# Kernel tuning notes

Hardware: AMD Instinct MI355X
Metric: run time of the kernel (lower is better)

Reference implementation:

```python
import jax, jax.numpy as jnp
import numpy as np

B, S, D, H = 2, 2048, 1024, 16
HD = D // H
DFF = 4096
EPS = 1e-5


def layernorm(x, w, b):
    m = jnp.mean(x, axis=-1, keepdims=True)
    v = jnp.mean((x - m) ** 2, axis=-1, keepdims=True)
    return (x - m) / jnp.sqrt(v + EPS) * w + b


def setup_inputs() -> dict:
    key = jax.random.key(0)
    ks = jax.random.split(key, 5)
    s = 0.02  # init scale for weights
    return {
        "src": jax.random.normal(ks[0], (B, S, D), jnp.float32),
        "norm_w": jnp.ones((D,), jnp.float32),
        "norm_b": jnp.zeros((D,), jnp.float32),
        "wqkv_w": jax.random.normal(ks[1], (D, 3 * D), jnp.float32) * s,
        "wqkv_b": jnp.zeros((3 * D,), jnp.float32),
        "out_w": jax.random.normal(ks[2], (D, D), jnp.float32) * s,
        "out_b": jnp.zeros((D,), jnp.float32),
        "fnorm_w": jnp.ones((D,), jnp.float32),
        "fnorm_b": jnp.zeros((D,), jnp.float32),
        "ff1_w": jax.random.normal(ks[3], (D, DFF), jnp.float32) * s,
        "ff1_b": jnp.zeros((DFF,), jnp.float32),
        "ff2_w": jax.random.normal(ks[4], (DFF, D), jnp.float32) * s,
        "ff2_b": jnp.zeros((D,), jnp.float32),
    }


def reference(src, norm_w, norm_b, wqkv_w, wqkv_b, out_w, out_b,
              fnorm_w, fnorm_b, ff1_w, ff1_b, ff2_w, ff2_b):
    bs, seq, dim = src.shape
    hd = dim // H
    qkv = layernorm(src, norm_w, norm_b) @ wqkv_w + wqkv_b  # [b,s,3d]
    qkv = qkv.reshape(bs, seq, 3, H, hd).transpose(2, 0, 3, 1, 4)  # [3,b,h,s,hd]
    q, k, v = qkv[0], qkv[1], qkv[2]
    # ALiBi bias: (j - i) * 2^{-h}, -inf above diagonal (causal)
    i = jnp.arange(seq)[:, None]
    j = jnp.arange(seq)[None, :]
    slopes = 2.0 ** (-jnp.arange(H, dtype=jnp.float32))  # [h]
    rel = (j - i).astype(jnp.float32)  # [s,s]
    bias = slopes[:, None, None] * rel[None]  # [h,s,s]
    bias = jnp.where((j > i)[None], -jnp.inf, bias)
    scale = 1.0 / jnp.sqrt(jnp.asarray(hd, jnp.float32))
    scores = jnp.einsum("bhqd,bhkd->bhqk", q, k) * scale + bias[None]
    attn = jax.nn.softmax(scores, axis=-1)
    ctx = jnp.einsum("bhqk,bhkd->bhqd", attn, v)
    ctx = ctx.transpose(0, 2, 1, 3).reshape(bs, seq, dim)
    src = src + ctx @ out_w + out_b
    h = layernorm(src, fnorm_w, fnorm_b)
    ff = jax.nn.relu(h @ ff1_w + ff1_b) @ ff2_w + ff2_b
    return src + ff
```

## Files before the change

kernel.cpp:

```cpp
#include <hip/hip_runtime.h>
#include <math.h>

#define S_   2048
#define D_   1024
#define H_   16
#define DFF_ 4096

#define NEGINF (-__builtin_huge_valf())

typedef __bf16 bf16x8 __attribute__((ext_vector_type(8)));
typedef __bf16 bf16x4 __attribute__((ext_vector_type(4)));
typedef float  f32x4  __attribute__((ext_vector_type(4)));

static __device__ __forceinline__ unsigned short f2bf_rne(float f) {
    unsigned int u = __float_as_uint(f);
    u = (u + 0x7fffu + ((u >> 16) & 1u)) >> 16;
    return (unsigned short)u;
}

template<bool OBF>
__global__ __launch_bounds__(256) void ln_kernel(
    const float* __restrict__ x, const float* __restrict__ w,
    const float* __restrict__ b, void* __restrict__ y)
{
    const int row = blockIdx.x;
    const int t = threadIdx.x;
    const float4 v = reinterpret_cast<const float4*>(x + (size_t)row * D_)[t];
    float s  = v.x + v.y + v.z + v.w;
    float ss = v.x*v.x + v.y*v.y + v.z*v.z + v.w*v.w;
    #pragma unroll
    for (int o = 32; o; o >>= 1) {
        s  += __shfl_xor(s,  o, 64);
        ss += __shfl_xor(ss, o, 64);
    }
    __shared__ float red[8];
    const int wid = t >> 6, lane = t & 63;
    if (lane == 0) { red[wid] = s; red[4 + wid] = ss; }
    __syncthreads();
    s  = red[0] + red[1] + red[2] + red[3];
    ss = red[4] + red[5] + red[6] + red[7];
    const float mean = s * (1.f / D_);
    const float var  = ss * (1.f / D_) - mean * mean;
    const float rstd = rsqrtf(var + 1e-5f);
    const float4 wv = reinterpret_cast<const float4*>(w)[t];
    const float4 bv = reinterpret_cast<const float4*>(b)[t];
    float4 o;
    o.x = (v.x - mean) * rstd * wv.x + bv.x;
    o.y = (v.y - mean) * rstd * wv.y + bv.y;
    o.z = (v.z - mean) * rstd * wv.z + bv.z;
    o.w = (v.w - mean) * rstd * wv.w + bv.w;
    if (OBF) {
        ushort4 o4;
        o4.x = f2bf_rne(o.x); o4.y = f2bf_rne(o.y);
        o4.z = f2bf_rne(o.z); o4.w = f2bf_rne(o.w);
        reinterpret_cast<ushort4*>((unsigned short*)y + (size_t)row * D_)[t] = o4;
    } else {
        reinterpret_cast<float4*>((float*)y + (size_t)row * D_)[t] = o;
    }
}

__global__ __launch_bounds__(256) void wcast_kernel(
    const float* __restrict__ in, unsigned short* __restrict__ outT, int K, int N)
{
    __shared__ float t[64][65];
    const int n0 = blockIdx.x * 64, k0 = blockIdx.y * 64;
    const int tid = threadIdx.x;
    #pragma unroll
    for (int i = 0; i < 16; ++i) {
        const int idx = i * 256 + tid;
        const int kk = idx >> 6, nn = idx & 63;
        t[kk][nn] = in[(size_t)(k0 + kk) * N + n0 + nn];
    }
    __syncthreads();
    #pragma unroll
    for (int i = 0; i < 16; ++i) {
        const int idx = i * 256 + tid;
        const int nn = idx >> 6, kk = idx & 63;
        outT[(size_t)(n0 + nn) * K + k0 + kk] = f2bf_rne(t[kk][nn]);
    }
}

template<int EPI, bool OBF, int BN>
__global__ __launch_bounds__(256) void bgemm_kernel(
    const __bf16* __restrict__ A,
    const __bf16* __restrict__ Bt,
    const float* __restrict__ bias, const float* __restrict__ res,
    void* __restrict__ Cv, int M, int N, int K)
{
    constexpr int B_IT = BN / 32;
    constexpr int MI   = (BN == 128) ? 4 : 2;
    __shared__ __align__(16) __bf16 As[2][128 * 64];
    __shared__ __align__(16) __bf16 Bs[2][BN * 64];
    const int tid  = threadIdx.x;
    const int w    = tid >> 6, lane = tid & 63;
    const int wrow0 = (BN == 128) ? (w >> 1) * 64 : w * 32;
    const int wcol0 = (BN == 128) ? (w & 1) * 64 : 0;

    const int nwg  = gridDim.x;
    const int lin  = blockIdx.x;
    const int wg   = (lin & 7) * (nwg >> 3) + (lin >> 3);
    const int gridM = M >> 7;
    const int col0 = (wg / gridM) * BN;
    const int row0 = (wg % gridM) << 7;

    const int srow = lane >> 3;
    const int scol = ((lane & 7) ^ srow) << 3;
    const int frow = lane & 15;
    const int l4   = lane >> 4;
    const int r7   = frow & 7;

    const __bf16* Abase = A  + (size_t)(row0 + srow) * K + scol;
    const __bf16* Bbase = Bt + (size_t)(col0 + srow) * K + scol;

    f32x4 acc[MI][4] = {};
    const int nt = K >> 6;

#define STAGE_G(bufi, kt)                                                              \
    _Pragma("unroll")                                                                  \
    for (int it = 0; it < 4; ++it) {                                                   \
        const int arow = w * 32 + it * 8;                                              \
        __builtin_amdgcn_global_load_lds(                                              \
            (__attribute__((address_space(1))) void*)(Abase + (size_t)arow * K + (kt)),\
            (__attribute__((address_space(3))) void*)(&As[bufi][arow * 64]), 16, 0, 0);\
    }                                                                                  \
    _Pragma("unroll")                                                                  \
    for (int it = 0; it < B_IT; ++it) {                                                \
        const int brow = w * (BN / 4) + it * 8;                                        \
        __builtin_amdgcn_global_load_lds(                                              \
            (__attribute__((address_space(1))) void*)(Bbase + (size_t)brow * K + (kt)),\
            (__attribute__((address_space(3))) void*)(&Bs[bufi][brow * 64]), 16, 0, 0);\
    }

    STAGE_G(0, 0)
    int buf = 0;
    for (int t = 0; t < nt; ++t) {
        __syncthreads();
        if (t + 1 < nt) {
            STAGE_G(buf ^ 1, (t + 1) << 6)
        }
        #pragma unroll
        for (int kk = 0; kk < 2; ++kk) {
            const int ch = ((kk * 4 + l4) ^ r7) * 8;
            bf16x8 af[MI], bfr[4];
            #pragma unroll
            for (int i = 0; i < MI; ++i)
                af[i] = *(const bf16x8*)&As[buf][(wrow0 + i * 16 + frow) * 64 + ch];
            #pragma unroll
            for (int i = 0; i < 4; ++i)
                bfr[i] = *(const bf16x8*)&Bs[buf][(wcol0 + i * 16 + frow) * 64 + ch];
            #pragma unroll
            for (int mi = 0; mi < MI; ++mi)
                #pragma unroll
                for (int ni = 0; ni < 4; ++ni)
                    acc[mi][ni] = __builtin_amdgcn_mfma_f32_16x16x32_bf16(
                        af[mi], bfr[ni], acc[mi][ni], 0, 0, 0);
        }
        buf ^= 1;
    }
#undef STAGE_G

    float bz[4];
    #pragma unroll
    for (int ni = 0; ni < 4; ++ni) bz[ni] = bias[col0 + wcol0 + ni * 16 + frow];
    #pragma unroll
    for (int mi = 0; mi < MI; ++mi) {
        #pragma unroll
        for (int j = 0; j < 4; ++j) {
            const int row = row0 + wrow0 + mi * 16 + l4 * 4 + j;
            #pragma unroll
            for (int ni = 0; ni < 4; ++ni) {
                const int col = col0 + wcol0 + ni * 16 + frow;
                float v = acc[mi][ni][j] + bz[ni];
                if (EPI == 1) v = fmaxf(v, 0.f);
                if (EPI == 2) v += res[(size_t)row * N + col];
                if (OBF) ((unsigned short*)Cv)[(size_t)row * N + col] = f2bf_rne(v);
                else     ((float*)Cv)[(size_t)row * N + col] = v;
            }
        }
    }
}

__global__ __launch_bounds__(256) void attn_kernel(
    const __bf16* __restrict__ qkv, __bf16* __restrict__ ctx)
{
    const int bh   = blockIdx.x & 31;
    const int qt   = 31 - (blockIdx.x >> 5);
    const int b    = bh >> 4, h = bh & 15;
    const int tid  = threadIdx.x;
    const int wid  = tid >> 6, lane = tid & 63;
    const int l15  = lane & 15, l4 = lane >> 4;
    const float slope2 = exp2f(-(float)h) * 1.44269504f;
    const size_t rowb = (size_t)b * S_;

    __shared__ __align__(16) __bf16 Ks[64 * 72];
    __shared__ __align__(16) __bf16 Vt[64 * 72];
    __shared__ __align__(16) __bf16 Ps[4 * 16 * 72];

    const int jr = tid >> 3;
    const int c  = tid & 7;
    const int c8 = c * 8;
    __bf16* psw = &Ps[wid * 16 * 72];
    const __bf16* base = qkv + rowb * 3072 + h * 64;

    const int i0 = qt << 6;

    bf16x8 qf[2];
    {
        const float QSC = 0.125f * 1.44269504f;
        const __bf16* qp = base + (size_t)(i0 + wid * 16 + l15) * 3072 + l4 * 8;
        bf16x8 r0 = *(const bf16x8*)(qp);
        bf16x8 r1 = *(const bf16x8*)(qp + 32);
        #pragma unroll
        for (int e = 0; e < 8; ++e) {
            qf[0][e] = (__bf16)((float)r0[e] * QSC);
            qf[1][e] = (__bf16)((float)r1[e] * QSC);
        }
    }

    float cb[4][4];
    #pragma unroll
    for (int ni = 0; ni < 4; ++ni)
        #pragma unroll
        for (int j = 0; j < 4; ++j)
            cb[ni][j] = slope2 * (float)(ni * 16 + l4 * 4 + j - wid * 16 - l15);

    float lsum = 0.f;
    f32x4 acc[4];
    #pragma unroll
    for (int ni = 0; ni < 4; ++ni) acc[ni] = (f32x4){0.f, 0.f, 0.f, 0.f};

    bf16x8 k0, k1, v0, v1;
    {
        const __bf16* kvp = base + (size_t)jr * 3072;
        k0 = *(const bf16x8*)(kvp + 1024 + c8);
        v0 = *(const bf16x8*)(kvp + 2048 + c8);
        k1 = *(const bf16x8*)(kvp + 32 * 3072 + 1024 + c8);
        v1 = *(const bf16x8*)(kvp + 32 * 3072 + 2048 + c8);
    }

    for (int kt = 0; kt <= qt; ++kt) {
        __syncthreads();
        *(bf16x8*)&Ks[jr * 72 + c8]        = k0;
        *(bf16x8*)&Ks[(jr + 32) * 72 + c8] = k1;
        const int sw0 = (((jr >> 3) ^ c) & 7) * 8 + (jr & 7);
        const int sw1 = ((((jr + 32) >> 3) ^ c) & 7) * 8 + (jr & 7);
        #pragma unroll
        for (int e = 0; e < 8; ++e) {
            Vt[(c8 + e) * 72 + sw0] = v0[e];
            Vt[(c8 + e) * 72 + sw1] = v1[e];
        }
        __syncthreads();

        if (kt < qt) {
            const __bf16* kvp = base + (size_t)(((kt + 1) << 6) + jr) * 3072;
            k0 = *(const bf16x8*)(kvp + 1024 + c8);
            v0 = *(const bf16x8*)(kvp + 2048 + c8);
            k1 = *(const bf16x8*)(kvp + 32 * 3072 + 1024 + c8);
            v1 = *(const bf16x8*)(kvp + 32 * 3072 + 2048 + c8);
        }

        f32x4 sf[4];
        #pragma unroll
        for (int ni = 0; ni < 4; ++ni) sf[ni] = (f32x4){0.f, 0.f, 0.f, 0.f};
        #pragma unroll
        for (int kd = 0; kd < 2; ++kd)
            #pragma unroll
            for (int ni = 0; ni < 4; ++ni) {
                const bf16x8 kf = *(const bf16x8*)&Ks[(ni * 16 + l15) * 72 + kd * 32 + l4 * 8];
                sf[ni] = __builtin_amdgcn_mfma_f32_16x16x32_bf16(kf, qf[kd], sf[ni], 0, 0, 0);
            }

        float p[4][4];
        if (kt == qt) {
            #pragma unroll
            for (int ni = 0; ni < 4; ++ni)
                #pragma unroll
                for (int j = 0; j < 4; ++j) {
                    const float e = (cb[ni][j] > 0.f)
                        ? 0.f
                        : __builtin_amdgcn_exp2f(sf[ni][j] + cb[ni][j]);
                    p[ni][j] = e;
                    lsum += e;
                }
        } else {
            const float dstep = slope2 * (float)((kt << 6) - i0);
            #pragma unroll
            for (int ni = 0; ni < 4; ++ni)
                #pragma unroll
                for (int j = 0; j < 4; ++j) {
                    const float e = __builtin_amdgcn_exp2f(sf[ni][j] + (cb[ni][j] + dstep));
                    p[ni][j] = e;
                    lsum += e;
                }
        }

        #pragma unroll
        for (int ni = 0; ni < 4; ++ni) {
            bf16x4 pk;
            pk[0] = (__bf16)p[ni][0]; pk[1] = (__bf16)p[ni][1];
            pk[2] = (__bf16)p[ni][2]; pk[3] = (__bf16)p[ni][3];
            *(bf16x4*)&psw[l15 * 72 + ni * 16 + l4 * 4] = pk;
        }
        asm volatile("" ::: "memory");

        #pragma unroll
        for (int kk = 0; kk < 2; ++kk) {
            const bf16x8 pa = *(const bf16x8*)&psw[l15 * 72 + kk * 32 + l4 * 8];
            #pragma unroll
            for (int ni = 0; ni < 4; ++ni) {
                const int d = ni * 16 + l15;
                const int pc = ((kk * 4 + l4) ^ (d >> 3)) & 7;
                const bf16x8 bv = *(const bf16x8*)&Vt[d * 72 + pc * 8];
                acc[ni] = __builtin_amdgcn_mfma_f32_16x16x32_bf16(pa, bv, acc[ni], 0, 0, 0);
            }
        }
    }

    lsum += __shfl_xor(lsum, 16, 64);
    lsum += __shfl_xor(lsum, 32, 64);
    float linv[4];
    #pragma unroll
    for (int j = 0; j < 4; ++j)
        linv[j] = 1.f / __shfl(lsum, l4 * 4 + j, 64);

    #pragma unroll
    for (int ni = 0; ni < 4; ++ni) {
        const int col = h * 64 + ni * 16 + l15;
        #pragma unroll
        for (int j = 0; j < 4; ++j) {
            const int row = i0 + wid * 16 + l4 * 4 + j;
            ctx[(rowb + row) * (size_t)D_ + col] = (__bf16)(acc[ni][j] * linv[j]);
        }
    }
}

extern "C" void kernel_launch(void* const* d_in, const int* in_sizes, int n_in,
                              void* d_out, int out_size, void* d_ws, size_t ws_size,
                              hipStream_t stream) {
    const float* src     = (const float*)d_in[0];
    const float* norm_w  = (const float*)d_in[1];
    const float* norm_b  = (const float*)d_in[2];
    const float* wqkv_w  = (const float*)d_in[3];
    const float* wqkv_b  = (const float*)d_in[4];
    const float* out_w   = (const float*)d_in[5];
    const float* out_b   = (const float*)d_in[6];
    const float* fnorm_w = (const float*)d_in[7];
    const float* fnorm_b = (const float*)d_in[8];
    const float* ff1_w   = (const float*)d_in[9];
    const float* ff1_b   = (const float*)d_in[10];
    const float* ff2_w   = (const float*)d_in[11];
    const float* ff2_b   = (const float*)d_in[12];
    float* out = (float*)d_out;

    const int M = 2 * S_;
    const size_t MB = 1u << 20;
    char* W = (char*)d_ws;
    unsigned short* wqkvT = (unsigned short*)(W);
    unsigned short* outT  = (unsigned short*)(W + 6  * MB);
    unsigned short* ff1T  = (unsigned short*)(W + 8  * MB);
    unsigned short* ff2T  = (unsigned short*)(W + 16 * MB);
    unsigned short* h1    = (unsigned short*)(W + 24 * MB);
    unsigned short* qkv   = (unsigned short*)(W + 32 * MB);
    unsigned short* ctx   = (unsigned short*)(W + 24 * MB);
    unsigned short* h2    = (unsigned short*)(W + 32 * MB);
    unsigned short* ffmid = (unsigned short*)(W + 40 * MB);
    float*          src2  = (float*)        (W + 80 * MB);

    wcast_kernel<<<dim3(3072/64, 1024/64), 256, 0, stream>>>(wqkv_w, wqkvT, 1024, 3072);
    wcast_kernel<<<dim3(1024/64, 1024/64), 256, 0, stream>>>(out_w,  outT,  1024, 1024);
    wcast_kernel<<<dim3(4096/64, 1024/64), 256, 0, stream>>>(ff1_w,  ff1T,  1024, 4096);
    wcast_kernel<<<dim3(1024/64, 4096/64), 256, 0, stream>>>(ff2_w,  ff2T,  4096, 1024);

    ln_kernel<true><<<M, 256, 0, stream>>>(src, norm_w, norm_b, h1);
    bgemm_kernel<0, true, 128><<<(3072/128) * (M/128), 256, 0, stream>>>(
        (const __bf16*)h1, (const __bf16*)wqkvT, wqkv_b, nullptr, qkv, M, 3072, 1024);
    attn_kernel<<<1024, 256, 0, stream>>>((const __bf16*)qkv, (__bf16*)ctx);
    bgemm_kernel<2, false, 64><<<(1024/64) * (M/128), 256, 0, stream>>>(
        (const __bf16*)ctx, (const __bf16*)outT, out_b, src, src2, M, 1024, 1024);
    ln_kernel<true><<<M, 256, 0, stream>>>(src2, fnorm_w, fnorm_b, h2);
    bgemm_kernel<1, true, 128><<<(4096/128) * (M/128), 256, 0, stream>>>(
        (const __bf16*)h2, (const __bf16*)ff1T, ff1_b, nullptr, ffmid, M, 4096, 1024);
    bgemm_kernel<2, false, 64><<<(1024/64) * (M/128), 256, 0, stream>>>(
        (const __bf16*)ffmid, (const __bf16*)ff2T, ff2_b, src2, out, M, 1024, 4096);
}
```

Before: 344.5 us.

## Split-K the FF2 GEMM with reduction kernel and use BK=32 for wide GEMMs

The final FF2 GEMM (K=4096) now runs as a two-way split-K. Each half writes fp32 partials, and a separate ksum kernel adds the partials, the residual and the bias. This doubles the workgroup count so more CUs are busy. The GEMM kernel is also templated on the K-tile size, with BK=32 and an adjusted LDS swizzle used for the QKV and FF1 GEMMs, which cuts LDS use per block. The cost is extra fp32 traffic for the partials and one more kernel launch.

```diff
diff --git a/kernel.cpp b/kernel.cpp
--- a/kernel.cpp
+++ b/kernel.cpp
@@ -80,74 +80,89 @@
     }
 }
 
-template<int EPI, bool OBF, int BN>
+template<int EPI, bool OBF, int BN, int BK>
 __global__ __launch_bounds__(256) void bgemm_kernel(
     const __bf16* __restrict__ A,
     const __bf16* __restrict__ Bt,
     const float* __restrict__ bias, const float* __restrict__ res,
     void* __restrict__ Cv, int M, int N, int K)
 {
-    constexpr int B_IT = BN / 32;
-    constexpr int MI   = (BN == 128) ? 4 : 2;
-    __shared__ __align__(16) __bf16 As[2][128 * 64];
-    __shared__ __align__(16) __bf16 Bs[2][BN * 64];
+    constexpr int RPI = 512 / BK;
+    constexpr int NCH = BK / 8;
+    constexpr int AIT = 32 / RPI;
+    constexpr int BIT = (BN / 4) / RPI;
+    constexpr int MI  = (BN == 128) ? 4 : 2;
+    constexpr int KKN = BK / 32;
+
+    __shared__ __align__(16) __bf16 As[2][128 * BK];
+    __shared__ __align__(16) __bf16 Bs[2][BN * BK];
     const int tid  = threadIdx.x;
     const int w    = tid >> 6, lane = tid & 63;
     const int wrow0 = (BN == 128) ? (w >> 1) * 64 : w * 32;
     const int wcol0 = (BN == 128) ? (w & 1) * 64 : 0;
 
-    const int nwg  = gridDim.x;
-    const int lin  = blockIdx.x;
-    const int wg   = (lin & 7) * (nwg >> 3) + (lin >> 3);
+    const int lin = blockIdx.x;
+    const int wg_full = (lin & 7) * (gridDim.x >> 3) + (lin >> 3);
+    int wg = wg_full, ks = 0;
+    if (EPI == 3) {
+        const int half = gridDim.x >> 1;
+        ks = wg_full >= half;
+        wg = wg_full - ks * half;
+    }
     const int gridM = M >> 7;
     const int col0 = (wg / gridM) * BN;
     const int row0 = (wg % gridM) << 7;
-
-    const int srow = lane >> 3;
-    const int scol = ((lane & 7) ^ srow) << 3;
-    const int frow = lane & 15;
-    const int l4   = lane >> 4;
-    const int r7   = frow & 7;
-
-    const __bf16* Abase = A  + (size_t)(row0 + srow) * K + scol;
-    const __bf16* Bbase = Bt + (size_t)(col0 + srow) * K + scol;
+    const int Keff  = (EPI == 3) ? (K >> 1) : K;
+    const int kbase = ks * Keff;
+
+    const int srow   = lane / NCH;
+    const int schunk = lane % NCH;
+    const int swk_s  = (BK == 64) ? (srow & 7) : ((srow >> 1) & 3);
+    const int scol   = (schunk ^ swk_s) * 8;
+    const int frow   = lane & 15;
+    const int l4     = lane >> 4;
+    const int swk_r  = (BK == 64) ? (frow & 7) : ((frow >> 1) & 3);
+
+    const __bf16* Abase = A  + (size_t)(row0 + srow) * K + kbase + scol;
+    const __bf16* Bbase = Bt + (size_t)(col0 + srow) * K + kbase + scol;
 
     f32x4 acc[MI][4] = {};
-    const int nt = K >> 6;
-
-#define STAGE_G(bufi, kt)                                                              \
-    _Pragma("unroll")                                                                  \
-    for (int it = 0; it < 4; ++it) {                                                   \
-        const int arow = w * 32 + it * 8;                                              \
-        __builtin_amdgcn_global_load_lds(                                              \
-            (__attribute__((address_space(1))) void*)(Abase + (size_t)arow * K + (kt)),\
-            (__attribute__((address_space(3))) void*)(&As[bufi][arow * 64]), 16, 0, 0);\
-    }                                                                                  \
-    _Pragma("unroll")                                                                  \
-    for (int it = 0; it < B_IT; ++it) {                                                \
-        const int brow = w * (BN / 4) + it * 8;                                        \
-        __builtin_amdgcn_global_load_lds(                                              \
-            (__attribute__((address_space(1))) void*)(Bbase + (size_t)brow * K + (kt)),\
-            (__attribute__((address_space(3))) void*)(&Bs[bufi][brow * 64]), 16, 0, 0);\
-    }
-
-    STAGE_G(0, 0)
+    const int nt = Keff / BK;
+
+    auto STAGE = [&](int bufi, int kt) {
+        #pragma unroll
+        for (int it = 0; it < AIT; ++it) {
+            const int arow = w * 32 + it * RPI;
+            __builtin_amdgcn_global_load_lds(
+                (__attribute__((address_space(1))) void*)(Abase + (size_t)arow * K + kt),
+                (__attribute__((address_space(3))) void*)(&As[bufi][arow * BK]), 16, 0, 0);
+        }
+        #pragma unroll
+        for (int it = 0; it < BIT; ++it) {
+            const int brow = w * (BN / 4) + it * RPI;
+            __builtin_amdgcn_global_load_lds(
+                (__attribute__((address_space(1))) void*)(Bbase + (size_t)brow * K + kt),
+                (__attribute__((address_space(3))) void*)(&Bs[bufi][brow * BK]), 16, 0, 0);
+        }
+    };
+
+    STAGE(0, 0);
     int buf = 0;
     for (int t = 0; t < nt; ++t) {
         __syncthreads();
         if (t + 1 < nt) {
-            STAGE_G(buf ^ 1, (t + 1) << 6)
-        }
-        #pragma unroll
-        for (int kk = 0; kk < 2; ++kk) {
-            const int ch = ((kk * 4 + l4) ^ r7) * 8;
+            STAGE(buf ^ 1, (t + 1) * BK);
+        }
+        #pragma unroll
+        for (int kk = 0; kk < KKN; ++kk) {
+            const int ch = ((kk * 4 + l4) ^ swk_r) * 8;
             bf16x8 af[MI], bfr[4];
             #pragma unroll
             for (int i = 0; i < MI; ++i)
-                af[i] = *(const bf16x8*)&As[buf][(wrow0 + i * 16 + frow) * 64 + ch];
+                af[i] = *(const bf16x8*)&As[buf][(wrow0 + i * 16 + frow) * BK + ch];
             #pragma unroll
             for (int i = 0; i < 4; ++i)
-                bfr[i] = *(const bf16x8*)&Bs[buf][(wcol0 + i * 16 + frow) * 64 + ch];
+                bfr[i] = *(const bf16x8*)&Bs[buf][(wcol0 + i * 16 + frow) * BK + ch];
             #pragma unroll
             for (int mi = 0; mi < MI; ++mi)
                 #pragma unroll
@@ -157,11 +172,13 @@
         }
         buf ^= 1;
     }
-#undef STAGE_G
-
-    float bz[4];
-    #pragma unroll
-    for (int ni = 0; ni < 4; ++ni) bz[ni] = bias[col0 + wcol0 + ni * 16 + frow];
+
+    float bz[4] = {0.f, 0.f, 0.f, 0.f};
+    if (EPI != 3) {
+        #pragma unroll
+        for (int ni = 0; ni < 4; ++ni) bz[ni] = bias[col0 + wcol0 + ni * 16 + frow];
+    }
+    float* Cd = (EPI == 3) ? (ks ? (float*)res : (float*)Cv) : (float*)Cv;
     #pragma unroll
     for (int mi = 0; mi < MI; ++mi) {
         #pragma unroll
@@ -173,10 +190,32 @@
                 float v = acc[mi][ni][j] + bz[ni];
                 if (EPI == 1) v = fmaxf(v, 0.f);
                 if (EPI == 2) v += res[(size_t)row * N + col];
-                if (OBF) ((unsigned short*)Cv)[(size_t)row * N + col] = f2bf_rne(v);
-                else     ((float*)Cv)[(size_t)row * N + col] = v;
+                if (EPI == 3) Cd[(size_t)row * N + col] = v;
+                else if (OBF) ((unsigned short*)Cv)[(size_t)row * N + col] = f2bf_rne(v);
+                else          ((float*)Cv)[(size_t)row * N + col] = v;
             }
         }
+    }
+}
+
+__global__ __launch_bounds__(256) void ksum_kernel(
+    const float* __restrict__ p0, const float* __restrict__ p1,
+    const float* __restrict__ s2, const float* __restrict__ bias,
+    float* __restrict__ out)
+{
+    const int total = 4096 * 1024 / 4;
+    const int stride = gridDim.x * 256;
+    for (int i = blockIdx.x * 256 + threadIdx.x; i < total; i += stride) {
+        const float4 a  = ((const float4*)p0)[i];
+        const float4 b  = ((const float4*)p1)[i];
+        const float4 s  = ((const float4*)s2)[i];
+        const float4 bs = ((const float4*)bias)[i & 255];
+        float4 o;
+        o.x = s.x + a.x + b.x + bs.x;
+        o.y = s.y + a.y + b.y + bs.y;
+        o.z = s.z + a.z + b.z + bs.z;
+        o.w = s.w + a.w + b.w + bs.w;
+        ((float4*)out)[i] = o;
     }
 }
 
@@ -365,6 +404,8 @@
     unsigned short* h2    = (unsigned short*)(W + 32 * MB);
     unsigned short* ffmid = (unsigned short*)(W + 40 * MB);
     float*          src2  = (float*)        (W + 80 * MB);
+    float*          p0    = (float*)        (W + 24 * MB);
+    float*          p1    = (float*)        (W + 96 * MB);
 
     wcast_kernel<<<dim3(3072/64, 1024/64), 256, 0, stream>>>(wqkv_w, wqkvT, 1024, 3072);
     wcast_kernel<<<dim3(1024/64, 1024/64), 256, 0, stream>>>(out_w,  outT,  1024, 1024);
@@ -372,14 +413,15 @@
     wcast_kernel<<<dim3(1024/64, 4096/64), 256, 0, stream>>>(ff2_w,  ff2T,  4096, 1024);
 
     ln_kernel<true><<<M, 256, 0, stream>>>(src, norm_w, norm_b, h1);
-    bgemm_kernel<0, true, 128><<<(3072/128) * (M/128), 256, 0, stream>>>(
+    bgemm_kernel<0, true, 128, 32><<<(3072/128) * (M/128), 256, 0, stream>>>(
         (const __bf16*)h1, (const __bf16*)wqkvT, wqkv_b, nullptr, qkv, M, 3072, 1024);
     attn_kernel<<<1024, 256, 0, stream>>>((const __bf16*)qkv, (__bf16*)ctx);
-    bgemm_kernel<2, false, 64><<<(1024/64) * (M/128), 256, 0, stream>>>(
+    bgemm_kernel<2, false, 64, 64><<<(1024/64) * (M/128), 256, 0, stream>>>(
         (const __bf16*)ctx, (const __bf16*)outT, out_b, src, src2, M, 1024, 1024);
     ln_kernel<true><<<M, 256, 0, stream>>>(src2, fnorm_w, fnorm_b, h2);
-    bgemm_kernel<1, true, 128><<<(4096/128) * (M/128), 256, 0, stream>>>(
+    bgemm_kernel<1, true, 128, 32><<<(4096/128) * (M/128), 256, 0, stream>>>(
         (const __bf16*)h2, (const __bf16*)ff1T, ff1_b, nullptr, ffmid, M, 4096, 1024);
-    bgemm_kernel<2, false, 64><<<(1024/64) * (M/128), 256, 0, stream>>>(
-        (const __bf16*)ffmid, (const __bf16*)ff2T, ff2_b, src2, out, M, 1024, 4096);
-}
+    bgemm_kernel<3, false, 64, 64><<<2 * (1024/64) * (M/128), 256, 0, stream>>>(
+        (const __bf16*)ffmid, (const __bf16*)ff2T, nullptr, p1, p0, M, 1024, 4096);
+    ksum_kernel<<<2048, 256, 0, stream>>>(p0, p1, src2, ff2_b, out);
+}
```

New measurement: 354.5 us. 2.9% more time.
